# Kernel tuning notes

Measured on AMD Instinct MI355X. Metric: run time of the kernel, lower is better.

Reference implementation:

```python
import jax, jax.numpy as jnp
import numpy as np
from jax import lax

FACTOR = 2  # fixed down-sampling factor in StyleGAN2 conv_downsample_2d
RESAMPLE_KERNEL = [1, 3, 3, 1]


def _setup_kernel(k):
    # StyleGAN2 _setup_kernel: separable 1D -> 2D outer product, normalized to sum 1
    k = np.asarray(k, dtype=np.float32)
    if k.ndim == 1:
        k = np.outer(k, k)
    k /= k.sum()
    return k


def setup_inputs() -> dict:
    key = jax.random.key(0)
    k1, k2 = jax.random.split(key)
    images = jax.random.normal(k1, (4, 128, 512, 512), dtype=jnp.float32)  # NCHW
    # equalised_weights: use_w_scale=True, lr_mult=1 -> init_std = 1.0; runtime_coeff
    # is computed in build() but never applied in call(), so weights are used raw.
    w = jax.random.normal(k2, (1, 1, 128, 256), dtype=jnp.float32)  # HWIO [kh,kw,inC,outC]
    return {"images": images, "w": w}


def reference(images, w):
    # conv_downsample_2d(x, w, k=[1,3,3,1], factor=2, gain=1), NCHW:
    #   k2d = setup(k) * gain
    #   p = (len2d(k) - factor) + (convW - 1); pad0=(p+1)//2, pad1=p//2
    #   x = upfirdn2d(x, k2d, up=1, down=1, pad0, pad1)  # per-channel FIR
    #   out = conv2d(x, w, strides=factor, padding='VALID')
    k2d = _setup_kernel(RESAMPLE_KERNEL)  # [4,4], gain=1
    kh = k2d.shape[0]
    convw = w.shape[1]
    p = (kh - FACTOR) + (convw - 1)
    pad0, pad1 = (p + 1) // 2, p // 2

    C = images.shape[1]
    # upfirdn applies true convolution with k2d == correlation with spatially flipped k2d
    fir = jnp.asarray(k2d[::-1, ::-1])[:, :, None, None]          # [kh,kw,1,1]
    fir = jnp.broadcast_to(fir, (kh, kh, 1, C)).astype(images.dtype)  # depthwise HWIO
    x = lax.conv_general_dilated(
        images, fir,
        window_strides=(1, 1),
        padding=[(pad0, pad1), (pad0, pad1)],
        dimension_numbers=("NCHW", "HWIO", "NCHW"),
        feature_group_count=C,
    )
    out = lax.conv_general_dilated(
        x, w,
        window_strides=(FACTOR, FACTOR),
        padding="VALID",
        dimension_numbers=("NCHW", "HWIO", "NCHW"),
    )
    return out  # [4, 256, 256, 256]
```

## Files before the change

kernel.cpp:

```cpp
#include <hip/hip_runtime.h>


#define VS 35

__global__ __launch_bounds__(512)
void fused_downconv_v7(const float* __restrict__ x, const float* __restrict__ w,
                       float* __restrict__ out) {
    __shared__ __align__(16) float v_s[2 * 8 * 4 * VS];

    const int tid  = threadIdx.x;
    const int lane = tid & 63;
    const int wv   = tid >> 6;
    const int oc0  = __builtin_amdgcn_readfirstlane((tid >> 6) << 5);

    const int ow0 = blockIdx.x * 16;
    const int oh0 = blockIdx.y * 4;
    const int n   = blockIdx.z;

    const int rbase = 2 * oh0 - 1;
    const int cbase = 2 * ow0 - 1;

    int off[10];
    unsigned ldmask = 0;
    {
        int gc = cbase + lane;
        bool cok = (lane < 34) && ((unsigned)gc < 512u);
        #pragma unroll
        for (int k = 0; k < 10; k++) {
            int gr = rbase + k;
            bool ok = cok && ((unsigned)gr < 512u);
            off[k] = ok ? (gr * 512 + gc) : 0;
            if (ok) ldmask |= 1u << k;
        }
    }

    const int owl = lane & 15;
    const int ohl = lane >> 4;

    float xr[10];
    float acc[32];
    #pragma unroll
    for (int i = 0; i < 32; i++) acc[i] = 0.f;

    auto prefetch = [&](int c0) {
        const float* xb = x + ((size_t)(n * 128 + c0 + wv)) * 262144;
        #pragma unroll
        for (int k = 0; k < 10; k++)
            xr[k] = ((ldmask >> k) & 1u) ? xb[off[k]] : 0.f;
    };
    auto vwrite = [&](int buf) {
        if (lane < 34) {
            #pragma unroll
            for (int o = 0; o < 4; o++) {
                float v = 0.125f * (xr[2 * o] + xr[2 * o + 3])
                        + 0.375f * (xr[2 * o + 1] + xr[2 * o + 2]);
                v_s[((buf * 8 + wv) * 4 + o) * VS + lane] = v;
            }
        }
    };

    prefetch(0);
    vwrite(0);
    prefetch(8);
    __syncthreads();

    for (int t = 0; t < 16; t++) {
        const int buf = t & 1;
        if (t < 15) {
            vwrite(buf ^ 1);
            if (t < 14) prefetch((t + 2) * 8);
        }
        #pragma unroll
        for (int cc = 0; cc < 8; cc++) {
            const float* vp = &v_s[((buf * 8 + cc) * 4 + ohl) * VS + 2 * owl];
            float v0 = vp[0], v1 = vp[1], v2 = vp[2], v3 = vp[3];
            float y = 0.125f * (v0 + v3) + 0.375f * (v1 + v2);
            const float* wrow = w + ((t * 8 + cc) << 8) + oc0;
            #pragma unroll
            for (int i = 0; i < 32; i++)
                acc[i] = fmaf(wrow[i], y, acc[i]);
        }
        __syncthreads();
    }

    {
        size_t base = (((size_t)n * 256 + oc0) * 256 + (size_t)(oh0 + ohl)) * 256
                      + ow0 + owl;
        #pragma unroll
        for (int i = 0; i < 32; i++)
            out[base + (size_t)i * 65536] = acc[i];
    }
}

extern "C" void kernel_launch(void* const* d_in, const int* in_sizes, int n_in,
                              void* d_out, int out_size, void* d_ws, size_t ws_size,
                              hipStream_t stream) {
    const float* x = (const float*)d_in[0];
    const float* w = (const float*)d_in[1];
    float* out = (float*)d_out;

    dim3 grid(16, 64, 4);
    dim3 block(512);
    hipLaunchKernelGGL(fused_downconv_v7, grid, block, 0, stream, x, w, out);
}
```

Before: 411.7 us.

## Double-buffer register prefetch to keep two channel groups of loads in flight

```diff
diff --git a/kernel.cpp b/kernel.cpp
--- a/kernel.cpp
+++ b/kernel.cpp
@@ -4,7 +4,7 @@
 #define VS 35
 
 __global__ __launch_bounds__(512)
-void fused_downconv_v7(const float* __restrict__ x, const float* __restrict__ w,
+void fused_downconv_v8(const float* __restrict__ x, const float* __restrict__ w,
                        float* __restrict__ out) {
     __shared__ __align__(16) float v_s[2 * 8 * 4 * VS];
 
@@ -20,35 +20,36 @@
     const int rbase = 2 * oh0 - 1;
     const int cbase = 2 * ow0 - 1;
 
-    int off[10];
-    unsigned ldmask = 0;
-    {
-        int gc = cbase + lane;
-        bool cok = (lane < 34) && ((unsigned)gc < 512u);
-        #pragma unroll
-        for (int k = 0; k < 10; k++) {
-            int gr = rbase + k;
-            bool ok = cok && ((unsigned)gr < 512u);
-            off[k] = ok ? (gr * 512 + gc) : 0;
-            if (ok) ldmask |= 1u << k;
-        }
+    const int gc   = cbase + lane;
+    const bool cok = (lane < 34) && ((unsigned)gc < 512u);
+    const int gcc  = min(max(gc, 0), 511);
+    int rowoff[10];
+    unsigned rmask = 0;
+    #pragma unroll
+    for (int k = 0; k < 10; k++) {
+        int gr = rbase + k;
+        rowoff[k] = min(max(gr, 0), 511) * 512;
+        if ((unsigned)gr < 512u) rmask |= (1u << k);
     }
+    const unsigned lmask = cok ? rmask : 0u;
 
     const int owl = lane & 15;
     const int ohl = lane >> 4;
 
-    float xr[10];
+    float xrA[10], xrB[10];
     float acc[32];
     #pragma unroll
     for (int i = 0; i < 32; i++) acc[i] = 0.f;
 
-    auto prefetch = [&](int c0) {
-        const float* xb = x + ((size_t)(n * 128 + c0 + wv)) * 262144;
+    auto prefetch = [&](float (&xr)[10], int c0) {
+        const float* xb = x + ((size_t)(n * 128 + c0 + wv)) * 262144 + gcc;
         #pragma unroll
-        for (int k = 0; k < 10; k++)
-            xr[k] = ((ldmask >> k) & 1u) ? xb[off[k]] : 0.f;
+        for (int k = 0; k < 10; k++) {
+            float v = xb[rowoff[k]];
+            xr[k] = ((lmask >> k) & 1u) ? v : 0.f;
+        }
     };
-    auto vwrite = [&](int buf) {
+    auto vwrite = [&](float (&xr)[10], int buf) {
         if (lane < 34) {
             #pragma unroll
             for (int o = 0; o < 4; o++) {
@@ -58,28 +59,34 @@
             }
         }
     };
-
-    prefetch(0);
-    vwrite(0);
-    prefetch(8);
-    __syncthreads();
-
-    for (int t = 0; t < 16; t++) {
-        const int buf = t & 1;
-        if (t < 15) {
-            vwrite(buf ^ 1);
-            if (t < 14) prefetch((t + 2) * 8);
-        }
+    auto gemm = [&](int buf, int ch) {
         #pragma unroll
         for (int cc = 0; cc < 8; cc++) {
             const float* vp = &v_s[((buf * 8 + cc) * 4 + ohl) * VS + 2 * owl];
             float v0 = vp[0], v1 = vp[1], v2 = vp[2], v3 = vp[3];
             float y = 0.125f * (v0 + v3) + 0.375f * (v1 + v2);
-            const float* wrow = w + ((t * 8 + cc) << 8) + oc0;
+            const float* wrow = w + ((ch * 8 + cc) << 8) + oc0;
             #pragma unroll
             for (int i = 0; i < 32; i++)
                 acc[i] = fmaf(wrow[i], y, acc[i]);
         }
+    };
+
+    prefetch(xrA, 0);
+    vwrite(xrA, 0);
+    prefetch(xrA, 8);
+    prefetch(xrB, 16);
+    __syncthreads();
+
+    for (int tt = 0; tt < 8; tt++) {
+        const int t0 = 2 * tt, t1 = 2 * tt + 1;
+        vwrite(xrA, 1);
+        if (tt < 7) prefetch(xrA, 8 * (t0 + 3));
+        gemm(0, t0);
+        __syncthreads();
+        if (tt < 7) vwrite(xrB, 0);
+        if (tt < 6) prefetch(xrB, 8 * (t1 + 3));
+        gemm(1, t1);
         __syncthreads();
     }
 
@@ -101,5 +108,5 @@
 
     dim3 grid(16, 64, 4);
     dim3 block(512);
-    hipLaunchKernelGGL(fused_downconv_v7, grid, block, 0, stream, x, w, out);
+    hipLaunchKernelGGL(fused_downconv_v8, grid, block, 0, stream, x, w, out);
 }
```

After: 596.5 us. 1.45x slower.

## Split fused FIR+conv into separate FIR pass and GEMM pass via workspace

Applied to the files above, without the earlier changes.

```diff
diff --git a/kernel.cpp b/kernel.cpp
--- a/kernel.cpp
+++ b/kernel.cpp
@@ -1,11 +1,93 @@
 #include <hip/hip_runtime.h>
 
 
-#define VS 35
+typedef __attribute__((ext_vector_type(4))) float f32x4;
+
+__global__ __launch_bounds__(256)
+void fir_pass(const float* __restrict__ x, float* __restrict__ y) {
+    __shared__ float vlds[8][516];
+
+    const int tid = threadIdx.x;
+    const int b   = blockIdx.x;
+    const int gh  = b & 31;
+    const int nc  = b >> 5;
+
+    const float* xim = x + (size_t)nc * 262144;
+
+    if (tid < 8)       vlds[tid][0]   = 0.f;
+    else if (tid < 16) vlds[tid - 8][513] = 0.f;
+
+    const int col = tid & 255;
+    const bool interior = (gh >= 1) && (gh <= 30);
+
+    #pragma unroll
+    for (int ohl = 0; ohl < 8; ohl++) {
+        const int rb = 2 * (gh * 8 + ohl) - 1;
+        #pragma unroll
+        for (int h = 0; h < 2; h++) {
+            const int c2 = col + h * 256;
+            float s0, s1, s2, s3;
+            if (interior) {
+                const float* p = xim + (size_t)rb * 512 + c2;
+                s0 = p[0]; s1 = p[512]; s2 = p[1024]; s3 = p[1536];
+            } else {
+                s0 = ((unsigned)(rb + 0) < 512u) ? xim[(size_t)(rb + 0) * 512 + c2] : 0.f;
+                s1 = ((unsigned)(rb + 1) < 512u) ? xim[(size_t)(rb + 1) * 512 + c2] : 0.f;
+                s2 = ((unsigned)(rb + 2) < 512u) ? xim[(size_t)(rb + 2) * 512 + c2] : 0.f;
+                s3 = ((unsigned)(rb + 3) < 512u) ? xim[(size_t)(rb + 3) * 512 + c2] : 0.f;
+            }
+            vlds[ohl][1 + c2] = 0.125f * (s0 + s3) + 0.375f * (s1 + s2);
+        }
+    }
+    __syncthreads();
+
+    const int ohl = tid >> 5;
+    const int owb = tid & 31;
+    float* yrow = y + ((size_t)nc * 256 + (size_t)(gh * 8 + ohl)) * 256;
+    #pragma unroll
+    for (int j = 0; j < 8; j++) {
+        const int ow = owb + 32 * j;
+        const float* vb = &vlds[ohl][2 * ow];
+        yrow[ow] = 0.125f * (vb[0] + vb[3]) + 0.375f * (vb[1] + vb[2]);
+    }
+}
 
 __global__ __launch_bounds__(512)
-void fused_downconv_v7(const float* __restrict__ x, const float* __restrict__ w,
-                       float* __restrict__ out) {
+void gemm_pass(const float* __restrict__ yws, const float* __restrict__ w,
+               float* __restrict__ out) {
+    const int tid  = threadIdx.x;
+    const int lane = tid & 63;
+    const int oc0  = __builtin_amdgcn_readfirstlane((tid >> 6) << 5);
+
+    const int n    = blockIdx.y;
+    const int ohw0 = blockIdx.x * 64;
+
+    const float* yb = yws + ((size_t)n * 128) * 65536 + ohw0 + lane;
+    const float* wb = w + oc0;
+
+    float acc[32];
+    #pragma unroll
+    for (int i = 0; i < 32; i++) acc[i] = 0.f;
+
+    #pragma unroll 8
+    for (int c = 0; c < 128; ++c) {
+        const float yv = yb[(size_t)c << 16];
+        const float* wr = wb + (c << 8);
+        #pragma unroll
+        for (int i = 0; i < 32; i++)
+            acc[i] = fmaf(wr[i], yv, acc[i]);
+    }
+
+    const size_t ob = ((size_t)n * 256 + oc0) * 65536 + ohw0 + lane;
+    #pragma unroll
+    for (int i = 0; i < 32; i++)
+        out[ob + (size_t)i * 65536] = acc[i];
+}
+
+#define VS 35
+__global__ __launch_bounds__(512)
+void fused_fallback(const float* __restrict__ x, const float* __restrict__ w,
+                    float* __restrict__ out) {
     __shared__ __align__(16) float v_s[2 * 8 * 4 * VS];
 
     const int tid  = threadIdx.x;
@@ -99,7 +181,14 @@
     const float* w = (const float*)d_in[1];
     float* out = (float*)d_out;
 
-    dim3 grid(16, 64, 4);
-    dim3 block(512);
-    hipLaunchKernelGGL(fused_downconv_v7, grid, block, 0, stream, x, w, out);
+    const size_t need = 4ull * 128 * 256 * 256 * 4;
+    if (ws_size >= need) {
+        float* yws = (float*)d_ws;
+        hipLaunchKernelGGL(fir_pass, dim3(16384), dim3(256), 0, stream, x, yws);
+        hipLaunchKernelGGL(gemm_pass, dim3(1024, 4), dim3(512), 0, stream,
+                           yws, w, out);
+    } else {
+        hipLaunchKernelGGL(fused_fallback, dim3(16, 64, 4), dim3(512), 0, stream,
+                           x, w, out);
+    }
 }
```

Measured after the change: 360.0 us. 12.6% less time.
